# Optimization experiments

Measured on AMD Instinct MI355X. Metric: run time of the kernel, lower is better.

Reference implementation:

```python
import jax, jax.numpy as jnp
import numpy as np

B, N, IN_DIM, OUT_DIM, C = 8, 8192, 1024, 512, 64
TEMPERATURE = 1.0
LN_EPS = 1e-5


def setup_inputs() -> dict:
    key = jax.random.key(0)
    ks = jax.random.split(key, 6)
    node_embeddings = jax.random.normal(ks[0], (B, N, IN_DIM), dtype=jnp.float32)
    node_mask = jnp.zeros((B, N), dtype=bool)  # True => node is masked out
    # xavier_uniform for cluster_centers [C, OUT_DIM]
    lim_c = float(np.sqrt(6.0 / (C + OUT_DIM)))
    cluster_centers = jax.random.uniform(ks[1], (C, OUT_DIM), jnp.float32, -lim_c, lim_c)
    # nn.Linear default init (kaiming-uniform-ish bounds)
    lim_n = float(1.0 / np.sqrt(IN_DIM))
    W_node = jax.random.uniform(ks[2], (IN_DIM, OUT_DIM), jnp.float32, -lim_n, lim_n)
    b_node = jax.random.uniform(ks[3], (OUT_DIM,), jnp.float32, -lim_n, lim_n)
    lim_k = float(1.0 / np.sqrt(OUT_DIM))
    W_cluster = jax.random.uniform(ks[4], (OUT_DIM, OUT_DIM), jnp.float32, -lim_k, lim_k)
    b_cluster = jax.random.uniform(ks[5], (OUT_DIM,), jnp.float32, -lim_k, lim_k)
    ln_gamma = jnp.ones((OUT_DIM,), jnp.float32)
    ln_beta = jnp.zeros((OUT_DIM,), jnp.float32)
    return {
        "node_embeddings": node_embeddings,
        "node_mask": node_mask,
        "cluster_centers": cluster_centers,
        "W_node": W_node,
        "b_node": b_node,
        "W_cluster": W_cluster,
        "b_cluster": b_cluster,
        "ln_gamma": ln_gamma,
        "ln_beta": ln_beta,
    }


def reference(node_embeddings, node_mask, cluster_centers, W_node, b_node,
              W_cluster, b_cluster, ln_gamma, ln_beta):
    # node projection: [B, N, D]
    node_proj = jnp.einsum('bni,io->bno', node_embeddings, W_node) + b_node
    # projected cluster centers (batch-independent): [C, D]
    ccp = cluster_centers @ W_cluster + b_cluster
    # similarities: [B, C, N]
    sims = jnp.einsum('cd,bnd->bcn', ccp, node_proj) / TEMPERATURE
    sims = jnp.where(node_mask[:, None, :], -jnp.inf, sims)
    assignment_weights = jax.nn.softmax(sims, axis=-1)  # dropout is identity in eval
    # aggregate: [B, C, D], residual add of projected centers
    compressed = jnp.einsum('bcn,bnd->bcd', assignment_weights, node_proj) + ccp
    # LayerNorm over last dim
    mu = jnp.mean(compressed, axis=-1, keepdims=True)
    var = jnp.var(compressed, axis=-1, keepdims=True)
    compressed = (compressed - mu) * jax.lax.rsqrt(var + LN_EPS) * ln_gamma + ln_beta
    return compressed, assignment_weights
```

## Files before the change

### kernel.cpp

```cpp
#include <hip/hip_runtime.h>
#include <hip/hip_bf16.h>
#include <math.h>

#define Bn 8
#define Nn 8192
#define KIN 1024
#define DOUT 512
#define NC 64
#define LN_EPS 1e-5f

typedef short bf16x8 __attribute__((ext_vector_type(8)));
typedef short s8v __attribute__((ext_vector_type(8)));
typedef short s4v __attribute__((ext_vector_type(4)));
typedef float f32x4 __attribute__((ext_vector_type(4)));

__device__ __forceinline__ short f2bf(float f) {
    __hip_bfloat16 h = __float2bfloat16(f);
    return __builtin_bit_cast(short, h);
}

__device__ __forceinline__ void load_lds16(const void* g, void* l) {
    __builtin_amdgcn_global_load_lds(
        (const __attribute__((address_space(1))) unsigned int*)g,
        (__attribute__((address_space(3))) unsigned int*)l, 16, 0, 0);
}

__global__ __launch_bounds__(256) void k_prep_w(const float* __restrict__ W,
                                                short* __restrict__ Wt) {
    __shared__ short L[64 * 72];
    const int tid = threadIdx.x;
    const int kt = blockIdx.x >> 3, nt = blockIdx.x & 7;
    const int k0 = kt * 64, n0 = nt * 64;
    {
        int r = tid >> 2, c0 = (tid & 3) * 16;
        const float* g = W + (size_t)(k0 + r) * DOUT + n0 + c0;
        float4 a0 = *reinterpret_cast<const float4*>(g);
        float4 a1 = *reinterpret_cast<const float4*>(g + 4);
        float4 a2 = *reinterpret_cast<const float4*>(g + 8);
        float4 a3 = *reinterpret_cast<const float4*>(g + 12);
        s8v p0, p1;
        p0[0]=f2bf(a0.x); p0[1]=f2bf(a0.y); p0[2]=f2bf(a0.z); p0[3]=f2bf(a0.w);
        p0[4]=f2bf(a1.x); p0[5]=f2bf(a1.y); p0[6]=f2bf(a1.z); p0[7]=f2bf(a1.w);
        p1[0]=f2bf(a2.x); p1[1]=f2bf(a2.y); p1[2]=f2bf(a2.z); p1[3]=f2bf(a2.w);
        p1[4]=f2bf(a3.x); p1[5]=f2bf(a3.y); p1[6]=f2bf(a3.z); p1[7]=f2bf(a3.w);
        *reinterpret_cast<s8v*>(&L[r * 72 + c0]) = p0;
        *reinterpret_cast<s8v*>(&L[r * 72 + c0 + 8]) = p1;
    }
    __syncthreads();
    {
        int n = tid >> 2, kc = (tid & 3) * 16;
        s8v y0, y1;
#pragma unroll
        for (int j = 0; j < 8; ++j) y0[j] = L[(kc + j) * 72 + n];
#pragma unroll
        for (int j = 0; j < 8; ++j) y1[j] = L[(kc + 8 + j) * 72 + n];
        short* o = Wt + (size_t)(n0 + n) * KIN + k0 + kc;
        *reinterpret_cast<s8v*>(o) = y0;
        *reinterpret_cast<s8v*>(o + 8) = y1;
    }
}

__global__ __launch_bounds__(256) void k_prep_c(
    const float* __restrict__ cc, const float* __restrict__ Wc,
    const float* __restrict__ bc, float* __restrict__ ccp_f,
    short* __restrict__ ccp_bf) {
    __shared__ float ccs[512];
    const int tid = threadIdx.x, c = blockIdx.x;
    ccs[tid] = cc[c * DOUT + tid];
    ccs[tid + 256] = cc[c * DOUT + tid + 256];
    __syncthreads();
    float a0 = bc[tid], a1 = bc[tid + 256];
    for (int k = 0; k < DOUT; ++k) {
        float s = ccs[k];
        a0 += s * Wc[(size_t)k * DOUT + tid];
        a1 += s * Wc[(size_t)k * DOUT + tid + 256];
    }
    ccp_f[c * DOUT + tid] = a0;
    ccp_f[c * DOUT + tid + 256] = a1;
    ccp_bf[c * DOUT + tid] = f2bf(a0);
    ccp_bf[c * DOUT + tid + 256] = f2bf(a1);
}

__global__ __launch_bounds__(256, 2) void k_gemm1(
    const float* __restrict__ A, const short* __restrict__ Wt,
    const float* __restrict__ bias, short* __restrict__ proj,
    short* __restrict__ projT) {
    __shared__ short As[64 * 40];
    __shared__ short Bs[512 * 32];
    const int tid = threadIdx.x, lane = tid & 63, wv = tid >> 6;
    const int quad = lane >> 4, l15 = lane & 15;
    const int m0 = blockIdx.x * 64;

    f32x4 acc[4][8];
#pragma unroll
    for (int i = 0; i < 4; ++i)
#pragma unroll
        for (int j = 0; j < 8; ++j) acc[i][j] = (f32x4){0.f, 0.f, 0.f, 0.f};

    const int ar = tid >> 2;
    const int ac = (tid & 2) * 8;
    const int ac2 = (tid & 3) * 8;
    const float* Ag = A + (size_t)(m0 + ar) * KIN + ac2;

    for (int it = 0; it < KIN / 32; ++it) {
        const int k0 = it * 32;
        __syncthreads();
        {
            float4 a0 = *reinterpret_cast<const float4*>(Ag + k0);
            float4 a1 = *reinterpret_cast<const float4*>(Ag + k0 + 4);
            s8v p;
            p[0]=f2bf(a0.x); p[1]=f2bf(a0.y); p[2]=f2bf(a0.z); p[3]=f2bf(a0.w);
            p[4]=f2bf(a1.x); p[5]=f2bf(a1.y); p[6]=f2bf(a1.z); p[7]=f2bf(a1.w);
            *reinterpret_cast<s8v*>(&As[ar * 40 + ac2]) = p;
        }
#pragma unroll
        for (int i = 0; i < 8; ++i) {
            int c = i * 256 + tid;
            int n = c >> 2, kc = c & 3;
            load_lds16(Wt + (size_t)n * KIN + k0 + kc * 8,
                       Bs + (i * 256 + wv * 64) * 8);
        }
        __syncthreads();
        bf16x8 af[4], bfr[8];
#pragma unroll
        for (int mi = 0; mi < 4; ++mi)
            af[mi] = *reinterpret_cast<const bf16x8*>(&As[(mi * 16 + l15) * 40 + quad * 8]);
#pragma unroll
        for (int ni = 0; ni < 8; ++ni)
            bfr[ni] = *reinterpret_cast<const bf16x8*>(&Bs[(wv * 128 + ni * 16 + l15) * 32 + quad * 8]);
#pragma unroll
        for (int mi = 0; mi < 4; ++mi)
#pragma unroll
            for (int ni = 0; ni < 8; ++ni)
                acc[mi][ni] = __builtin_amdgcn_mfma_f32_16x16x32_bf16(af[mi], bfr[ni], acc[mi][ni], 0, 0, 0);
    }
#pragma unroll
    for (int ni = 0; ni < 8; ++ni) {
        int col = wv * 128 + ni * 16 + l15;
        float bv = bias[col];
#pragma unroll
        for (int mi = 0; mi < 4; ++mi) {
            int row0 = m0 + mi * 16 + quad * 4;
            s4v t;
#pragma unroll
            for (int r = 0; r < 4; ++r) {
                short v = f2bf(acc[mi][ni][r] + bv);
                t[r] = v;
                proj[(size_t)(row0 + r) * DOUT + col] = v;
            }
            *reinterpret_cast<s4v*>(projT + (size_t)col * (Bn * Nn) + row0) = t;
        }
    }
}

__global__ __launch_bounds__(256) void k_sims(
    const short* __restrict__ ccp_bf, const short* __restrict__ proj,
    float* __restrict__ sims) {
    __shared__ short As[64 * 32];
    __shared__ short Bs[128 * 32];
    const int tid = threadIdx.x, lane = tid & 63, wv = tid >> 6;
    const int quad = lane >> 4, l15 = lane & 15;
    const int b = blockIdx.x >> 6, nt = blockIdx.x & 63;
    const int n0 = nt * 128;
    const int wm = wv & 1, wn = wv >> 1;

    f32x4 acc[2][4];
#pragma unroll
    for (int i = 0; i < 2; ++i)
#pragma unroll
        for (int j = 0; j < 4; ++j) acc[i][j] = (f32x4){0.f, 0.f, 0.f, 0.f};

    for (int it = 0; it < DOUT / 32; ++it) {
        const int k0 = it * 32;
        __syncthreads();
        {
#pragma unroll
            for (int i = 0; i < 2; ++i) {
                int c = i * 256 + tid;
                int r = c >> 2, kc = c & 3;
                load_lds16(ccp_bf + (size_t)r * DOUT + k0 + kc * 8,
                           As + (i * 256 + wv * 64) * 8);
            }
        }
#pragma unroll
        for (int i = 0; i < 2; ++i) {
            int c = i * 256 + tid;
            int r = c >> 2, kc = c & 3;
            load_lds16(proj + (size_t)(b * Nn + n0 + r) * DOUT + k0 + kc * 8,
                       Bs + (i * 256 + wv * 64) * 8);
        }
        __syncthreads();
        bf16x8 af[2], bfr[4];
#pragma unroll
        for (int mi = 0; mi < 2; ++mi)
            af[mi] = *reinterpret_cast<const bf16x8*>(&As[(wm * 32 + mi * 16 + l15) * 32 + quad * 8]);
#pragma unroll
        for (int ni = 0; ni < 4; ++ni)
            bfr[ni] = *reinterpret_cast<const bf16x8*>(&Bs[(wn * 64 + ni * 16 + l15) * 32 + quad * 8]);
#pragma unroll
        for (int mi = 0; mi < 2; ++mi)
#pragma unroll
            for (int ni = 0; ni < 4; ++ni)
                acc[mi][ni] = __builtin_amdgcn_mfma_f32_16x16x32_bf16(af[mi], bfr[ni], acc[mi][ni], 0, 0, 0);
    }
#pragma unroll
    for (int mi = 0; mi < 2; ++mi)
#pragma unroll
        for (int ni = 0; ni < 4; ++ni)
#pragma unroll
            for (int r = 0; r < 4; ++r) {
                int c = wm * 32 + mi * 16 + quad * 4 + r;
                int n = n0 + wn * 64 + ni * 16 + l15;
                sims[((size_t)b * NC + c) * Nn + n] = acc[mi][ni][r];
            }
}

__global__ __launch_bounds__(256) void k_softmax(
    float* __restrict__ aw, const unsigned char* __restrict__ mask,
    short* __restrict__ aw_bf) {
    __shared__ float red[8];
    const int tid = threadIdx.x, lane = tid & 63, wv = tid >> 6;
    const int b = blockIdx.x >> 6, c = blockIdx.x & 63;
    float* p = aw + ((size_t)b * NC + c) * Nn;
    short* q = aw_bf + ((size_t)b * NC + c) * Nn;
    const unsigned char* mp = mask + b * Nn;

    float v[32];
    float mx = -INFINITY;
#pragma unroll
    for (int i = 0; i < 32; ++i) {
        int idx = tid + i * 256;
        float x = p[idx];
        if (mp[idx]) x = -INFINITY;
        v[i] = x;
        mx = fmaxf(mx, x);
    }
    for (int off = 32; off; off >>= 1) mx = fmaxf(mx, __shfl_xor(mx, off));
    if (lane == 0) red[wv] = mx;
    __syncthreads();
    mx = fmaxf(fmaxf(red[0], red[1]), fmaxf(red[2], red[3]));
    __syncthreads();

    float s = 0.f;
#pragma unroll
    for (int i = 0; i < 32; ++i) {
        v[i] = expf(v[i] - mx);
        s += v[i];
    }
    for (int off = 32; off; off >>= 1) s += __shfl_xor(s, off);
    if (lane == 0) red[wv] = s;
    __syncthreads();
    s = red[0] + red[1] + red[2] + red[3];
    float inv = 1.f / s;
#pragma unroll
    for (int i = 0; i < 32; ++i) {
        int idx = tid + i * 256;
        float w = v[i] * inv;
        p[idx] = w;
        q[idx] = f2bf(w);
    }
}

__global__ __launch_bounds__(256) void k_agg(
    const short* __restrict__ aw_bf, const short* __restrict__ projT,
    float* __restrict__ partial) {
    __shared__ short As[64 * 32];
    __shared__ short Bs[128 * 32];
    const int tid = threadIdx.x, lane = tid & 63, wv = tid >> 6;
    const int quad = lane >> 4, l15 = lane & 15;
    const int b = blockIdx.x >> 5, dt = (blockIdx.x >> 3) & 3, ks = blockIdx.x & 7;
    const int d0 = dt * 128;
    const int wm = wv & 1, wn = wv >> 1;

    f32x4 acc[2][4];
#pragma unroll
    for (int i = 0; i < 2; ++i)
#pragma unroll
        for (int j = 0; j < 4; ++j) acc[i][j] = (f32x4){0.f, 0.f, 0.f, 0.f};

    for (int it = 0; it < 32; ++it) {
        const int nb = ks * 1024 + it * 32;
        __syncthreads();
#pragma unroll
        for (int i = 0; i < 2; ++i) {
            int c = i * 256 + tid;
            int r = c >> 2, kc = c & 3;
            load_lds16(aw_bf + ((size_t)b * NC + r) * Nn + nb + kc * 8,
                       As + (i * 256 + wv * 64) * 8);
        }
#pragma unroll
        for (int i = 0; i < 2; ++i) {
            int c = i * 256 + tid;
            int r = c >> 2, kc = c & 3;
            load_lds16(projT + (size_t)(d0 + r) * (Bn * Nn) + b * Nn + nb + kc * 8,
                       Bs + (i * 256 + wv * 64) * 8);
        }
        __syncthreads();
        bf16x8 af[2], bfr[4];
#pragma unroll
        for (int mi = 0; mi < 2; ++mi)
            af[mi] = *reinterpret_cast<const bf16x8*>(&As[(wm * 32 + mi * 16 + l15) * 32 + quad * 8]);
#pragma unroll
        for (int ni = 0; ni < 4; ++ni)
            bfr[ni] = *reinterpret_cast<const bf16x8*>(&Bs[(wn * 64 + ni * 16 + l15) * 32 + quad * 8]);
#pragma unroll
        for (int mi = 0; mi < 2; ++mi)
#pragma unroll
            for (int ni = 0; ni < 4; ++ni)
                acc[mi][ni] = __builtin_amdgcn_mfma_f32_16x16x32_bf16(af[mi], bfr[ni], acc[mi][ni], 0, 0, 0);
    }
#pragma unroll
    for (int mi = 0; mi < 2; ++mi)
#pragma unroll
        for (int ni = 0; ni < 4; ++ni)
#pragma unroll
            for (int r = 0; r < 4; ++r) {
                int c = wm * 32 + mi * 16 + quad * 4 + r;
                int d = d0 + wn * 64 + ni * 16 + l15;
                partial[(((size_t)b * 8 + ks) * NC + c) * DOUT + d] = acc[mi][ni][r];
            }
}

__global__ __launch_bounds__(256) void k_ln(
    const float* __restrict__ partial, const float* __restrict__ ccp,
    const float* __restrict__ gamma, const float* __restrict__ beta,
    float* __restrict__ out) {
    __shared__ float red[16];
    const int tid = threadIdx.x, lane = tid & 63, wv = tid >> 6;
    const int b = blockIdx.x >> 6, c = blockIdx.x & 63;
    float v0 = ccp[c * DOUT + tid], v1 = ccp[c * DOUT + tid + 256];
#pragma unroll
    for (int ks = 0; ks < 8; ++ks) {
        const float* pp = partial + (((size_t)b * 8 + ks) * NC + c) * DOUT;
        v0 += pp[tid];
        v1 += pp[tid + 256];
    }
    float s = v0 + v1, sq = v0 * v0 + v1 * v1;
    for (int off = 32; off; off >>= 1) {
        s += __shfl_xor(s, off);
        sq += __shfl_xor(sq, off);
    }
    if (lane == 0) { red[wv] = s; red[8 + wv] = sq; }
    __syncthreads();
    s = red[0] + red[1] + red[2] + red[3];
    sq = red[8] + red[9] + red[10] + red[11];
    float mu = s * (1.f / 512.f);
    float var = sq * (1.f / 512.f) - mu * mu;
    float rs = rsqrtf(var + LN_EPS);
    size_t base = ((size_t)b * NC + c) * DOUT;
    out[base + tid] = (v0 - mu) * rs * gamma[tid] + beta[tid];
    out[base + tid + 256] = (v1 - mu) * rs * gamma[tid + 256] + beta[tid + 256];
}

extern "C" void kernel_launch(void* const* d_in, const int* in_sizes, int n_in,
                              void* d_out, int out_size, void* d_ws, size_t ws_size,
                              hipStream_t stream) {
    const float* node_emb = (const float*)d_in[0];
    const unsigned char* mask = (const unsigned char*)d_in[1];
    const float* cc = (const float*)d_in[2];
    const float* Wn = (const float*)d_in[3];
    const float* bn = (const float*)d_in[4];
    const float* Wc = (const float*)d_in[5];
    const float* bc = (const float*)d_in[6];
    const float* gamma = (const float*)d_in[7];
    const float* beta = (const float*)d_in[8];
    float* out = (float*)d_out;

    char* ws = (char*)d_ws;
    short* proj   = (short*)(ws);
    short* projT  = (short*)(ws + 67108864);
    short* aw_bf  = (short*)(ws + 134217728);
    float* ccp_f  = (float*)(ws + 142606336);
    short* ccp_bf = (short*)(ws + 142737408);
    short* Wt     = (short*)(ws + 142802944);
    float* partial= (float*)(ws + 143851520);

    float* sims = out + (size_t)Bn * NC * DOUT;

    k_prep_w<<<128, 256, 0, stream>>>(Wn, Wt);
    k_prep_c<<<64, 256, 0, stream>>>(cc, Wc, bc, ccp_f, ccp_bf);
    k_gemm1<<<1024, 256, 0, stream>>>(node_emb, Wt, bn, proj, projT);
    k_sims<<<512, 256, 0, stream>>>(ccp_bf, proj, sims);
    k_softmax<<<512, 256, 0, stream>>>(sims, mask, aw_bf);
    k_agg<<<256, 256, 0, stream>>>(aw_bf, projT, partial);
    k_ln<<<512, 256, 0, stream>>>(partial, ccp_f, gamma, beta, out);
}
```

Before: 567.6 us.

## Double-buffer LDS tiles in GEMM kernels and stage projT transpose via LDS

```diff
diff --git a/kernel.cpp b/kernel.cpp
--- a/kernel.cpp
+++ b/kernel.cpp
@@ -85,8 +85,9 @@
     const float* __restrict__ A, const short* __restrict__ Wt,
     const float* __restrict__ bias, short* __restrict__ proj,
     short* __restrict__ projT) {
-    __shared__ short As[64 * 40];
-    __shared__ short Bs[512 * 32];
+    __shared__ short smem[2 * 64 * 40 + 2 * 512 * 32];
+    short (*As)[64 * 40] = reinterpret_cast<short(*)[64 * 40]>(smem);
+    short (*Bs)[512 * 32] = reinterpret_cast<short(*)[512 * 32]>(smem + 2 * 64 * 40);
     const int tid = threadIdx.x, lane = tid & 63, wv = tid >> 6;
     const int quad = lane >> 4, l15 = lane & 15;
     const int m0 = blockIdx.x * 64;
@@ -98,66 +99,97 @@
         for (int j = 0; j < 8; ++j) acc[i][j] = (f32x4){0.f, 0.f, 0.f, 0.f};
 
     const int ar = tid >> 2;
-    const int ac = (tid & 2) * 8;
     const int ac2 = (tid & 3) * 8;
     const float* Ag = A + (size_t)(m0 + ar) * KIN + ac2;
 
+    {
+#pragma unroll
+        for (int i = 0; i < 8; ++i) {
+            int c = i * 256 + tid;
+            int n = c >> 2, kc = c & 3;
+            load_lds16(Wt + (size_t)n * KIN + kc * 8,
+                       &Bs[0][(i * 256 + wv * 64) * 8]);
+        }
+        float4 a0 = *reinterpret_cast<const float4*>(Ag);
+        float4 a1 = *reinterpret_cast<const float4*>(Ag + 4);
+        s8v p;
+        p[0]=f2bf(a0.x); p[1]=f2bf(a0.y); p[2]=f2bf(a0.z); p[3]=f2bf(a0.w);
+        p[4]=f2bf(a1.x); p[5]=f2bf(a1.y); p[6]=f2bf(a1.z); p[7]=f2bf(a1.w);
+        *reinterpret_cast<s8v*>(&As[0][ar * 40 + ac2]) = p;
+    }
+    __syncthreads();
+
+    int cur = 0;
     for (int it = 0; it < KIN / 32; ++it) {
-        const int k0 = it * 32;
-        __syncthreads();
-        {
-            float4 a0 = *reinterpret_cast<const float4*>(Ag + k0);
-            float4 a1 = *reinterpret_cast<const float4*>(Ag + k0 + 4);
+        const bool pf = (it + 1 < KIN / 32);
+        float4 a0, a1;
+        if (pf) {
+            const int k1 = (it + 1) * 32;
+            a0 = *reinterpret_cast<const float4*>(Ag + k1);
+            a1 = *reinterpret_cast<const float4*>(Ag + k1 + 4);
+#pragma unroll
+            for (int i = 0; i < 8; ++i) {
+                int c = i * 256 + tid;
+                int n = c >> 2, kc = c & 3;
+                load_lds16(Wt + (size_t)n * KIN + k1 + kc * 8,
+                           &Bs[cur ^ 1][(i * 256 + wv * 64) * 8]);
+            }
+        }
+        bf16x8 af[4], bfr[8];
+#pragma unroll
+        for (int mi = 0; mi < 4; ++mi)
+            af[mi] = *reinterpret_cast<const bf16x8*>(&As[cur][(mi * 16 + l15) * 40 + quad * 8]);
+#pragma unroll
+        for (int ni = 0; ni < 8; ++ni)
+            bfr[ni] = *reinterpret_cast<const bf16x8*>(&Bs[cur][(wv * 128 + ni * 16 + l15) * 32 + quad * 8]);
+#pragma unroll
+        for (int mi = 0; mi < 4; ++mi)
+#pragma unroll
+            for (int ni = 0; ni < 8; ++ni)
+                acc[mi][ni] = __builtin_amdgcn_mfma_f32_16x16x32_bf16(af[mi], bfr[ni], acc[mi][ni], 0, 0, 0);
+        if (pf) {
             s8v p;
             p[0]=f2bf(a0.x); p[1]=f2bf(a0.y); p[2]=f2bf(a0.z); p[3]=f2bf(a0.w);
             p[4]=f2bf(a1.x); p[5]=f2bf(a1.y); p[6]=f2bf(a1.z); p[7]=f2bf(a1.w);
-            *reinterpret_cast<s8v*>(&As[ar * 40 + ac2]) = p;
-        }
-#pragma unroll
-        for (int i = 0; i < 8; ++i) {
-            int c = i * 256 + tid;
-            int n = c >> 2, kc = c & 3;
-            load_lds16(Wt + (size_t)n * KIN + k0 + kc * 8,
-                       Bs + (i * 256 + wv * 64) * 8);
+            *reinterpret_cast<s8v*>(&As[cur ^ 1][ar * 40 + ac2]) = p;
         }
         __syncthreads();
-        bf16x8 af[4], bfr[8];
-#pragma unroll
-        for (int mi = 0; mi < 4; ++mi)
-            af[mi] = *reinterpret_cast<const bf16x8*>(&As[(mi * 16 + l15) * 40 + quad * 8]);
-#pragma unroll
-        for (int ni = 0; ni < 8; ++ni)
-            bfr[ni] = *reinterpret_cast<const bf16x8*>(&Bs[(wv * 128 + ni * 16 + l15) * 32 + quad * 8]);
-#pragma unroll
-        for (int mi = 0; mi < 4; ++mi)
-#pragma unroll
-            for (int ni = 0; ni < 8; ++ni)
-                acc[mi][ni] = __builtin_amdgcn_mfma_f32_16x16x32_bf16(af[mi], bfr[ni], acc[mi][ni], 0, 0, 0);
-    }
+        cur ^= 1;
+    }
+
+    short* T = smem;
 #pragma unroll
     for (int ni = 0; ni < 8; ++ni) {
         int col = wv * 128 + ni * 16 + l15;
         float bv = bias[col];
 #pragma unroll
         for (int mi = 0; mi < 4; ++mi) {
-            int row0 = m0 + mi * 16 + quad * 4;
+            int ml = mi * 16 + quad * 4;
             s4v t;
 #pragma unroll
             for (int r = 0; r < 4; ++r) {
                 short v = f2bf(acc[mi][ni][r] + bv);
                 t[r] = v;
-                proj[(size_t)(row0 + r) * DOUT + col] = v;
+                proj[(size_t)(m0 + ml + r) * DOUT + col] = v;
             }
-            *reinterpret_cast<s4v*>(projT + (size_t)col * (Bn * Nn) + row0) = t;
-        }
+            *reinterpret_cast<s4v*>(&T[col * 72 + ml]) = t;
+        }
+    }
+    __syncthreads();
+#pragma unroll
+    for (int p = 0; p < 16; ++p) {
+        int col = p * 32 + (tid >> 3);
+        int ch = (tid & 7) * 8;
+        s8v v = *reinterpret_cast<const s8v*>(&T[col * 72 + ch]);
+        *reinterpret_cast<s8v*>(projT + (size_t)col * (Bn * Nn) + m0 + ch) = v;
     }
 }
 
 __global__ __launch_bounds__(256) void k_sims(
     const short* __restrict__ ccp_bf, const short* __restrict__ proj,
     float* __restrict__ sims) {
-    __shared__ short As[64 * 32];
-    __shared__ short Bs[128 * 32];
+    __shared__ short As[2][64 * 32];
+    __shared__ short Bs[2][128 * 32];
     const int tid = threadIdx.x, lane = tid & 63, wv = tid >> 6;
     const int quad = lane >> 4, l15 = lane & 15;
     const int b = blockIdx.x >> 6, nt = blockIdx.x & 63;
@@ -170,38 +202,40 @@
 #pragma unroll
         for (int j = 0; j < 4; ++j) acc[i][j] = (f32x4){0.f, 0.f, 0.f, 0.f};
 
-    for (int it = 0; it < DOUT / 32; ++it) {
-        const int k0 = it * 32;
-        __syncthreads();
+    auto stage = [&](int buf, int k0) {
         {
-#pragma unroll
-            for (int i = 0; i < 2; ++i) {
-                int c = i * 256 + tid;
-                int r = c >> 2, kc = c & 3;
-                load_lds16(ccp_bf + (size_t)r * DOUT + k0 + kc * 8,
-                           As + (i * 256 + wv * 64) * 8);
-            }
+            int r = tid >> 2, kc = tid & 3;
+            load_lds16(ccp_bf + (size_t)r * DOUT + k0 + kc * 8,
+                       &As[buf][(wv * 64) * 8]);
         }
 #pragma unroll
         for (int i = 0; i < 2; ++i) {
             int c = i * 256 + tid;
             int r = c >> 2, kc = c & 3;
             load_lds16(proj + (size_t)(b * Nn + n0 + r) * DOUT + k0 + kc * 8,
-                       Bs + (i * 256 + wv * 64) * 8);
-        }
-        __syncthreads();
+                       &Bs[buf][(i * 256 + wv * 64) * 8]);
+        }
+    };
+
+    stage(0, 0);
+    __syncthreads();
+    int cur = 0;
+    for (int it = 0; it < DOUT / 32; ++it) {
+        if (it + 1 < DOUT / 32) stage(cur ^ 1, (it + 1) * 32);
         bf16x8 af[2], bfr[4];
 #pragma unroll
         for (int mi = 0; mi < 2; ++mi)
-            af[mi] = *reinterpret_cast<const bf16x8*>(&As[(wm * 32 + mi * 16 + l15) * 32 + quad * 8]);
+            af[mi] = *reinterpret_cast<const bf16x8*>(&As[cur][(wm * 32 + mi * 16 + l15) * 32 + quad * 8]);
 #pragma unroll
         for (int ni = 0; ni < 4; ++ni)
-            bfr[ni] = *reinterpret_cast<const bf16x8*>(&Bs[(wn * 64 + ni * 16 + l15) * 32 + quad * 8]);
+            bfr[ni] = *reinterpret_cast<const bf16x8*>(&Bs[cur][(wn * 64 + ni * 16 + l15) * 32 + quad * 8]);
 #pragma unroll
         for (int mi = 0; mi < 2; ++mi)
 #pragma unroll
             for (int ni = 0; ni < 4; ++ni)
                 acc[mi][ni] = __builtin_amdgcn_mfma_f32_16x16x32_bf16(af[mi], bfr[ni], acc[mi][ni], 0, 0, 0);
+        __syncthreads();
+        cur ^= 1;
     }
 #pragma unroll
     for (int mi = 0; mi < 2; ++mi)
@@ -264,11 +298,11 @@
 __global__ __launch_bounds__(256) void k_agg(
     const short* __restrict__ aw_bf, const short* __restrict__ projT,
     float* __restrict__ partial) {
-    __shared__ short As[64 * 32];
-    __shared__ short Bs[128 * 32];
+    __shared__ short As[2][64 * 32];
+    __shared__ short Bs[2][128 * 32];
     const int tid = threadIdx.x, lane = tid & 63, wv = tid >> 6;
     const int quad = lane >> 4, l15 = lane & 15;
-    const int b = blockIdx.x >> 5, dt = (blockIdx.x >> 3) & 3, ks = blockIdx.x & 7;
+    const int b = blockIdx.x >> 5, dt = (blockIdx.x >> 3) & 3, ksp = blockIdx.x & 7;
     const int d0 = dt * 128;
     const int wm = wv & 1, wn = wv >> 1;
 
@@ -278,36 +312,40 @@
 #pragma unroll
         for (int j = 0; j < 4; ++j) acc[i][j] = (f32x4){0.f, 0.f, 0.f, 0.f};
 
-    for (int it = 0; it < 32; ++it) {
-        const int nb = ks * 1024 + it * 32;
-        __syncthreads();
-#pragma unroll
-        for (int i = 0; i < 2; ++i) {
-            int c = i * 256 + tid;
-            int r = c >> 2, kc = c & 3;
+    auto stage = [&](int buf, int nb) {
+        {
+            int r = tid >> 2, kc = tid & 3;
             load_lds16(aw_bf + ((size_t)b * NC + r) * Nn + nb + kc * 8,
-                       As + (i * 256 + wv * 64) * 8);
+                       &As[buf][(wv * 64) * 8]);
         }
 #pragma unroll
         for (int i = 0; i < 2; ++i) {
             int c = i * 256 + tid;
             int r = c >> 2, kc = c & 3;
             load_lds16(projT + (size_t)(d0 + r) * (Bn * Nn) + b * Nn + nb + kc * 8,
-                       Bs + (i * 256 + wv * 64) * 8);
-        }
-        __syncthreads();
+                       &Bs[buf][(i * 256 + wv * 64) * 8]);
+        }
+    };
+
+    stage(0, ksp * 1024);
+    __syncthreads();
+    int cur = 0;
+    for (int it = 0; it < 32; ++it) {
+        if (it + 1 < 32) stage(cur ^ 1, ksp * 1024 + (it + 1) * 32);
         bf16x8 af[2], bfr[4];
 #pragma unroll
         for (int mi = 0; mi < 2; ++mi)
-            af[mi] = *reinterpret_cast<const bf16x8*>(&As[(wm * 32 + mi * 16 + l15) * 32 + quad * 8]);
+            af[mi] = *reinterpret_cast<const bf16x8*>(&As[cur][(wm * 32 + mi * 16 + l15) * 32 + quad * 8]);
 #pragma unroll
         for (int ni = 0; ni < 4; ++ni)
-            bfr[ni] = *reinterpret_cast<const bf16x8*>(&Bs[(wn * 64 + ni * 16 + l15) * 32 + quad * 8]);
+            bfr[ni] = *reinterpret_cast<const bf16x8*>(&Bs[cur][(wn * 64 + ni * 16 + l15) * 32 + quad * 8]);
 #pragma unroll
         for (int mi = 0; mi < 2; ++mi)
 #pragma unroll
             for (int ni = 0; ni < 4; ++ni)
                 acc[mi][ni] = __builtin_amdgcn_mfma_f32_16x16x32_bf16(af[mi], bfr[ni], acc[mi][ni], 0, 0, 0);
+        __syncthreads();
+        cur ^= 1;
     }
 #pragma unroll
     for (int mi = 0; mi < 2; ++mi)
@@ -317,7 +355,7 @@
             for (int r = 0; r < 4; ++r) {
                 int c = wm * 32 + mi * 16 + quad * 4 + r;
                 int d = d0 + wn * 64 + ni * 16 + l15;
-                partial[(((size_t)b * 8 + ks) * NC + c) * DOUT + d] = acc[mi][ni][r];
+                partial[(((size_t)b * 8 + ksp) * NC + c) * DOUT + d] = acc[mi][ni][r];
             }
 }
 
```

Measured after the change: 551.8 us. 2.8% less time.
